# Performance work log

Measured on AMD Instinct MI355X. Metric: run time of the kernel, lower is better.

The kernel has to match this reference:

```python
import jax, jax.numpy as jnp
import numpy as np

ARRAY_SIZE = 128   # crossbar rows
CBITS = 4          # psum ADC bits
LEV = 2 ** (CBITS - 1)
ALPHA = ARRAY_SIZE / LEV   # psum quant step
EPS = 1e-5

# ---- binary activation / weight quant with STE (hardtanh grad) ----
@jax.custom_vjp
def ste_sign(x):
    return jnp.where(x >= 0, 1.0, -1.0).astype(x.dtype)

def _sign_fwd(x):
    return ste_sign(x), x

def _sign_bwd(x, g):
    return (g * (jnp.abs(x) <= 1.0).astype(g.dtype),)

ste_sign.defvjp(_sign_fwd, _sign_bwd)

# ---- psum (partial-sum) quantization: cbits-level ADC over each crossbar array ----
@jax.custom_vjp
def psum_quant(p):
    return jnp.clip(jnp.round(p / ALPHA), -LEV, LEV - 1) * ALPHA

def _pq_fwd(p):
    return psum_quant(p), p

def _pq_bwd(p, g):
    return (g * (jnp.abs(p) <= ARRAY_SIZE).astype(g.dtype),)

psum_quant.defvjp(_pq_fwd, _pq_bwd)

# ---- layers ----
def bn(x, p):
    g, b, m, v = p  # each [C]
    sh = (1, -1) + (1,) * (x.ndim - 2)
    return (x - m.reshape(sh)) * (g.reshape(sh) / jnp.sqrt(v.reshape(sh) + EPS)) + b.reshape(sh)

def maxpool2(x):
    return jax.lax.reduce_window(x, -jnp.inf, jax.lax.max, (1, 1, 2, 2), (1, 1, 2, 2), 'VALID')

def conv_same(x, w):
    return jax.lax.conv_general_dilated(x, w, (1, 1), 'SAME')

def psum_conv(x, w):
    # crossbar-mapped conv: input channels split into groups of arraySize//(kh*kw),
    # each group conv'd separately, psum-quantized (ADC), then accumulated.
    O, Cin, kh, kw = w.shape
    chunk = max(1, ARRAY_SIZE // (kh * kw))
    G = -(-Cin // chunk)
    pad = G * chunk - Cin
    xp = jnp.pad(x, ((0, 0), (0, pad), (0, 0), (0, 0)))
    wp = jnp.pad(w, ((0, 0), (0, pad), (0, 0), (0, 0)))
    B, _, H, W = x.shape
    xg = xp.reshape(B, G, chunk, H, W).transpose(1, 0, 2, 3, 4)   # [G,B,c,H,W]
    wg = wp.reshape(O, G, chunk, kh, kw).transpose(1, 0, 2, 3, 4)  # [G,O,c,kh,kw]
    ps = jax.vmap(conv_same)(xg, wg)                               # [G,B,O,H,W]
    return psum_quant(ps).sum(0)

def psum_linear(x, w):
    # x [B,D], w [O,D]; D divisible by ARRAY_SIZE
    B, D = x.shape
    O = w.shape[0]
    G = D // ARRAY_SIZE
    ps = jnp.einsum('bgc,ogc->gbo', x.reshape(B, G, ARRAY_SIZE), w.reshape(O, G, ARRAY_SIZE))
    return psum_quant(ps).sum(0)


def setup_inputs() -> dict:
    key = jax.random.key(0)
    ks = iter(jax.random.split(key, 64))
    def nrm(shape, s=0.05):
        return jax.random.normal(next(ks), shape, jnp.float32) * s
    def bnp(C):
        return jnp.stack([jax.random.uniform(next(ks), (C,), jnp.float32) + 0.5,
                          nrm((C,), 0.1), nrm((C,), 0.1),
                          jax.random.uniform(next(ks), (C,), jnp.float32) + 0.5])
    return dict(
        x=jax.random.normal(next(ks), (64, 3, 32, 32), jnp.float32),
        conv0_w=nrm((128, 3, 3, 3)), bn0=bnp(128),
        w1=nrm((128, 128, 3, 3)), bn1=bnp(128),
        w2=nrm((256, 128, 3, 3)), bn2=bnp(256),
        w3=nrm((256, 256, 3, 3)), bn3=bnp(256),
        w4=nrm((512, 256, 3, 3)), bn4=bnp(512),
        w5=nrm((512, 512, 3, 3)), bn5=bnp(512),
        fc1_w=nrm((1024, 8192)), bnf1=bnp(1024),
        fc2_w=nrm((1024, 1024)), bnf2=bnp(1024),
        out_w=nrm((10, 1024)), out_b=nrm((10,)), bnout=bnp(10),
    )


def reference(x, conv0_w, bn0, w1, bn1, w2, bn2, w3, bn3, w4, bn4, w5, bn5,
              fc1_w, bnf1, fc2_w, bnf2, out_w, out_b, bnout):
    h = conv_same(x, conv0_w)                       # full-precision first conv
    h = ste_sign(bn(h, bn0))
    h = psum_conv(h, ste_sign(w1)); h = maxpool2(h); h = ste_sign(bn(h, bn1))
    h = psum_conv(h, ste_sign(w2)); h = ste_sign(bn(h, bn2))
    h = psum_conv(h, ste_sign(w3)); h = maxpool2(h); h = ste_sign(bn(h, bn3))
    h = psum_conv(h, ste_sign(w4)); h = ste_sign(bn(h, bn4))
    h = psum_conv(h, ste_sign(w5)); h = maxpool2(h); h = ste_sign(bn(h, bn5))
    h = h.reshape(h.shape[0], -1)                   # [B, 8192]
    h = ste_sign(bn(psum_linear(h, ste_sign(fc1_w)), bnf1))
    h = bn(psum_linear(h, ste_sign(fc2_w)), bnf2)   # abits=32 -> identity nonlinear
    h = h @ out_w.T + out_b
    return bn(h, bnout)
```

## Files before the change

kernel.cpp:

```cpp
#include <hip/hip_runtime.h>
#include <cstdint>
#include <cstddef>

using bf16x8 = __attribute__((ext_vector_type(8))) short;
using f32x4  = __attribute__((ext_vector_type(4))) float;
using u32x4  = __attribute__((ext_vector_type(4))) unsigned int;

#define DI __device__ __forceinline__

DI float pq3(float a) {
    return fminf(rintf(a), 7.f);
}
DI float pq16(float ps) {
    return fminf(rintf(ps * 0.0625f), 7.f) * 16.f;
}

DI float bnv(float x, float g, float b, float m, float v) {
    return (x - m) * (g / sqrtf(v + 1e-5f)) + b;
}

DI unsigned short sgn_bf16(float v) {
    return (v >= 0.f) ? (unsigned short)0x3F80 : (unsigned short)0xBF80;
}

__global__ __launch_bounds__(256)
void k_conv0(const float* __restrict__ x, const float* __restrict__ w,
             const float* __restrict__ bnp, unsigned short* __restrict__ out) {
    __shared__ float sX[3][3][36];
    const int b = blockIdx.x >> 5, y = blockIdx.x & 31;
    const int tid = threadIdx.x;
    const int o = tid & 127, xc = tid >> 7;

    for (int i = tid; i < 3 * 3 * 36; i += 256) {
        int col = i % 36, rr = (i / 36) % 3, c = i / 108;
        int gy = y + rr - 1, gx = col - 1;
        float v = 0.f;
        if ((unsigned)gy < 32u && (unsigned)gx < 32u)
            v = x[((b * 3 + c) * 32 + gy) * 32 + gx];
        sX[c][rr][col] = v;
    }
    float wr[27];
    const float* wp = w + o * 27;
    #pragma unroll
    for (int t = 0; t < 27; ++t) wr[t] = wp[t];
    __syncthreads();

    const float bg = bnp[o], bb = bnp[128 + o], bm = bnp[256 + o], bv = bnp[384 + o];
    unsigned short* op = out + ((size_t)(b * 32 + y) * 32) * 128 + o;

    #pragma unroll
    for (int q = 0; q < 4; ++q) {
        float acc0 = 0.f, acc1 = 0.f, acc2 = 0.f, acc3 = 0.f;
        const int X0 = xc * 16 + q * 4;
        #pragma unroll
        for (int c = 0; c < 3; ++c)
            #pragma unroll
            for (int ky = 0; ky < 3; ++ky) {
                float xv0 = sX[c][ky][X0 + 0], xv1 = sX[c][ky][X0 + 1];
                float xv2 = sX[c][ky][X0 + 2], xv3 = sX[c][ky][X0 + 3];
                float xv4 = sX[c][ky][X0 + 4], xv5 = sX[c][ky][X0 + 5];
                float w0 = wr[c * 9 + ky * 3 + 0];
                float w1 = wr[c * 9 + ky * 3 + 1];
                float w2 = wr[c * 9 + ky * 3 + 2];
                acc0 += xv0 * w0 + xv1 * w1 + xv2 * w2;
                acc1 += xv1 * w0 + xv2 * w1 + xv3 * w2;
                acc2 += xv2 * w0 + xv3 * w1 + xv4 * w2;
                acc3 += xv3 * w0 + xv4 * w1 + xv5 * w2;
            }
        op[(size_t)(X0 + 0) * 128] = sgn_bf16(bnv(acc0, bg, bb, bm, bv));
        op[(size_t)(X0 + 1) * 128] = sgn_bf16(bnv(acc1, bg, bb, bm, bv));
        op[(size_t)(X0 + 2) * 128] = sgn_bf16(bnv(acc2, bg, bb, bm, bv));
        op[(size_t)(X0 + 3) * 128] = sgn_bf16(bnv(acc3, bg, bb, bm, bv));
    }
}

__global__ __launch_bounds__(256)
void k_pack_w(const float* __restrict__ w, unsigned short* __restrict__ wpk,
              int Cin, int O, int G) {
    int idx = blockIdx.x * 256 + threadIdx.x;
    int total = G * O * 160;
    if (idx >= total) return;
    int c = idx & 15;
    int tap = (idx >> 4) % 10;
    int rest = idx / 160;
    int o = rest % O, g = rest / O;
    unsigned short v = 0;
    int cg = g * 14 + c;
    if (tap < 9 && c < 14 && cg < Cin)
        v = (w[((size_t)o * Cin + cg) * 9 + tap] >= 0.f) ? (unsigned short)0x3D80
                                                         : (unsigned short)0xBD80;
    wpk[idx] = v;
}

template <int H, int W, int Cin, int O, int G, int RH, int RW, int POOLMODE>
__global__ __launch_bounds__(256)
void k_conv_mfma(const unsigned int* __restrict__ act,
                 const unsigned short* __restrict__ wpk,
                 const float* __restrict__ bnp,
                 unsigned short* __restrict__ outa,
                 unsigned short* __restrict__ a5p,
                 const unsigned int* __restrict__ zbuf) {
    constexpr int SH = RH + 2, SW = RW + 2;
    constexpr int MS = RH * RW / 16;
    constexpr int NREGX = W / RW;
    constexpr int SLOT8 = SH * SW * 8;
    constexpr int NST = (SLOT8 + 255) / 256;
    static_assert(POOLMODE != 1 || RW == 16, "pool mode 1 needs RW=16");
    static_assert(POOLMODE != 2 || (RW == 8 && MS == 4), "pool mode 2 needs 8x8");

    __shared__ __align__(16) unsigned int sA[SH * SW * 12];

    const int tid  = threadIdx.x;
    const int regY = (int)blockIdx.x / NREGX, regX = (int)blockIdx.x % NREGX;
    const int o0   = blockIdx.y * 64;
    const int b    = blockIdx.z;

    const int lane = tid & 63, wv = tid >> 6;
    const int n  = lane & 15;
    const int kb = lane >> 4;
    const int hb = kb >> 1, ch = kb & 1;

    const unsigned int* sptr[NST];
    int sdst[NST];
    #pragma unroll
    for (int it = 0; it < NST; ++it) {
        int i = it * 256 + tid;
        sdst[it] = -1;
        if (i < SLOT8) {
            int cp = i & 7, slot = i >> 3;
            int yy = slot / SW, xx = slot - yy * SW;
            int gy = regY * RH + yy - 1, gx = regX * RW + xx - 1;
            sdst[it] = slot * 12 + (((cp >> 2) + slot) % 3) * 4 + (cp & 3);
            sptr[it] = ((unsigned)gy < (unsigned)H && (unsigned)gx < (unsigned)W)
                     ? act + ((size_t)(b * H + gy) * W + gx) * (Cin / 2) + cp
                     : zbuf + cp;
        }
    }

    int offMS[MS][5];
    #pragma unroll
    for (int ms = 0; ms < MS; ++ms) {
        int p = ms * 16 + n;
        int y = p / RW, x = p % RW;
        #pragma unroll
        for (int s = 0; s < 5; ++s) {
            int t = 2 * s + hb;
            int slotT = (t <= 8) ? ((y + t / 3) * SW + (x + t % 3)) : (y * SW + x);
            offMS[ms][s] = slotT * 48 + ((ch + slotT) % 3) * 16;
        }
    }

    float tot[MS][4];
    #pragma unroll
    for (int ms = 0; ms < MS; ++ms) {
        tot[ms][0] = 0.f; tot[ms][1] = 0.f; tot[ms][2] = 0.f; tot[ms][3] = 0.f;
    }

    const unsigned short* wg = wpk + ((size_t)o0 + wv * 16 + n) * 160 + ch * 8;

    #pragma unroll 1
    for (int g = 0; g < G; ++g) {
        #pragma unroll
        for (int it = 0; it < NST; ++it)
            if (sdst[it] >= 0) {
                sA[sdst[it]] = *sptr[it];
                sptr[it] += 7;
            }
        bf16x8 bq[5];
        #pragma unroll
        for (int s = 0; s < 5; ++s) {
            int tap = 2 * s + hb;
            bq[s] = *(const bf16x8*)(wg + tap * 16);
        }
        wg += O * 160;
        __syncthreads();

        const char* sAc = (const char*)sA;
        #pragma unroll
        for (int ms = 0; ms < MS; ++ms) {
            f32x4 acc = {0.f, 0.f, 0.f, 0.f};
            #pragma unroll
            for (int s = 0; s < 5; ++s) {
                bf16x8 af = *(const bf16x8*)(sAc + offMS[ms][s]);
                acc = __builtin_amdgcn_mfma_f32_16x16x32_bf16(af, bq[s], acc, 0, 0, 0);
            }
            tot[ms][0] += pq3(acc[0]);
            tot[ms][1] += pq3(acc[1]);
            tot[ms][2] += pq3(acc[2]);
            tot[ms][3] += pq3(acc[3]);
        }
        __syncthreads();
    }

    const int oc = o0 + wv * 16 + n;
    const float bg = bnp[oc], bb = bnp[O + oc], bm = bnp[2 * O + oc], bvr = bnp[3 * O + oc];

    if constexpr (POOLMODE == 0) {
        #pragma unroll
        for (int ms = 0; ms < MS; ++ms)
            #pragma unroll
            for (int r = 0; r < 4; ++r) {
                int p = ms * 16 + 4 * kb + r;
                int y = regY * RH + p / RW, x = regX * RW + p % RW;
                float val = bnv(16.f * tot[ms][r], bg, bb, bm, bvr);
                outa[(((size_t)b * H + y) * W + x) * O + oc] = sgn_bf16(val);
            }
    } else if constexpr (POOLMODE == 1) {
        #pragma unroll
        for (int j = 0; j < MS / 2; ++j)
            #pragma unroll
            for (int q = 0; q < 2; ++q) {
                float v = fmaxf(fmaxf(tot[2 * j][2 * q], tot[2 * j][2 * q + 1]),
                                fmaxf(tot[2 * j + 1][2 * q], tot[2 * j + 1][2 * q + 1]));
                float val = bnv(16.f * v, bg, bb, bm, bvr);
                int py = regY * (RH / 2) + j, px = regX * (RW / 2) + 2 * kb + q;
                outa[(((size_t)b * (H / 2) + py) * (W / 2) + px) * O + oc] = sgn_bf16(val);
            }
    } else {
        #pragma unroll
        for (int ms = 0; ms < MS; ++ms)
            #pragma unroll
            for (int q = 0; q < 2; ++q) {
                float h = fmaxf(tot[ms][2 * q], tot[ms][2 * q + 1]);
                float o2 = __shfl_xor(h, 32);
                float v = fmaxf(h, o2);
                if (hb == 0) {
                    float val = bnv(16.f * v, bg, bb, bm, bvr);
                    int d = oc * 16 + ms * 4 + 2 * ch + q;
                    a5p[((size_t)(d >> 3) * 64 + b) * 8 + (d & 7)] = sgn_bf16(val);
                }
            }
    }
}

template <int D, int GPB>
__global__ __launch_bounds__(256)
void k_fc_mfma(const unsigned short* __restrict__ bpk, const float* __restrict__ w,
               float* __restrict__ accg) {
    const int lane = threadIdx.x & 63, wv = threadIdx.x >> 6;
    const int n = lane & 15, kb = lane >> 4;
    const int orow = blockIdx.x * 64 + wv * 16 + n;
    const int g0 = blockIdx.y * GPB;

    float tot[4][4];
    #pragma unroll
    for (int s = 0; s < 4; ++s)
        #pragma unroll
        for (int r = 0; r < 4; ++r) tot[s][r] = 0.f;

    #pragma unroll 1
    for (int g = 0; g < GPB; ++g) {
        const int kbase = (g0 + g) * 128;
        f32x4 a0 = {0,0,0,0}, a1 = {0,0,0,0}, a2 = {0,0,0,0}, a3 = {0,0,0,0};
        #pragma unroll
        for (int s = 0; s < 4; ++s) {
            const int k0 = kbase + s * 32 + kb * 8;
            const float* wp = w + (size_t)orow * D + k0;
            float4 wlo = *(const float4*)wp;
            float4 whi = *(const float4*)(wp + 4);
            bf16x8 af;
            af[0] = (short)sgn_bf16(wlo.x); af[1] = (short)sgn_bf16(wlo.y);
            af[2] = (short)sgn_bf16(wlo.z); af[3] = (short)sgn_bf16(wlo.w);
            af[4] = (short)sgn_bf16(whi.x); af[5] = (short)sgn_bf16(whi.y);
            af[6] = (short)sgn_bf16(whi.z); af[7] = (short)sgn_bf16(whi.w);
            const unsigned short* bp = bpk + (size_t)(k0 >> 3) * 512;
            bf16x8 b0 = *(const bf16x8*)(bp + (n +  0) * 8);
            bf16x8 b1 = *(const bf16x8*)(bp + (n + 16) * 8);
            bf16x8 b2 = *(const bf16x8*)(bp + (n + 32) * 8);
            bf16x8 b3 = *(const bf16x8*)(bp + (n + 48) * 8);
            a0 = __builtin_amdgcn_mfma_f32_16x16x32_bf16(af, b0, a0, 0, 0, 0);
            a1 = __builtin_amdgcn_mfma_f32_16x16x32_bf16(af, b1, a1, 0, 0, 0);
            a2 = __builtin_amdgcn_mfma_f32_16x16x32_bf16(af, b2, a2, 0, 0, 0);
            a3 = __builtin_amdgcn_mfma_f32_16x16x32_bf16(af, b3, a3, 0, 0, 0);
        }
        #pragma unroll
        for (int r = 0; r < 4; ++r) {
            tot[0][r] += pq16(a0[r]); tot[1][r] += pq16(a1[r]);
            tot[2][r] += pq16(a2[r]); tot[3][r] += pq16(a3[r]);
        }
    }
    const int od = blockIdx.x * 64 + wv * 16 + kb * 4;
    #pragma unroll
    for (int s = 0; s < 4; ++s)
        #pragma unroll
        for (int r = 0; r < 4; ++r)
            atomicAdd(&accg[(size_t)(od + r) * 64 + s * 16 + n], tot[s][r]);
}

template <bool SIGN>
__global__ __launch_bounds__(256)
void k_fc_ep(const float* __restrict__ accg, const float* __restrict__ bnp,
             unsigned short* __restrict__ packed, float* __restrict__ h2, int O) {
    int idx = blockIdx.x * 256 + threadIdx.x;
    int b = idx & 63, o = idx >> 6;
    float val = bnv(accg[idx], bnp[o], bnp[O + o], bnp[2 * O + o], bnp[3 * O + o]);
    if (SIGN) packed[((size_t)(o >> 3) * 64 + b) * 8 + (o & 7)] = sgn_bf16(val);
    else      h2[(size_t)b * 1024 + o] = val;
}

__global__ __launch_bounds__(64)
void k_out(const float* __restrict__ h2, const float* __restrict__ ow,
           const float* __restrict__ ob, const float* __restrict__ bnp,
           float* __restrict__ out) {
    int b = blockIdx.x / 10, o = blockIdx.x % 10;
    int lane = threadIdx.x;
    float acc = 0.f;
    #pragma unroll
    for (int i = 0; i < 16; ++i) {
        int k = i * 64 + lane;
        acc += h2[b * 1024 + k] * ow[o * 1024 + k];
    }
    #pragma unroll
    for (int off = 32; off; off >>= 1) acc += __shfl_xor(acc, off);
    if (lane == 0)
        out[b * 10 + o] = bnv(acc + ob[o], bnp[o], bnp[10 + o], bnp[20 + o], bnp[30 + o]);
}

extern "C" void kernel_launch(void* const* d_in, const int* in_sizes, int n_in,
                              void* d_out, int out_size, void* d_ws, size_t ws_size,
                              hipStream_t stream) {
    const float* x     = (const float*)d_in[0];
    const float* w0    = (const float*)d_in[1];
    const float* bn0   = (const float*)d_in[2];
    const float* w1    = (const float*)d_in[3];
    const float* bn1   = (const float*)d_in[4];
    const float* w2    = (const float*)d_in[5];
    const float* bn2   = (const float*)d_in[6];
    const float* w3    = (const float*)d_in[7];
    const float* bn3   = (const float*)d_in[8];
    const float* w4    = (const float*)d_in[9];
    const float* bn4   = (const float*)d_in[10];
    const float* w5    = (const float*)d_in[11];
    const float* bn5   = (const float*)d_in[12];
    const float* fc1w  = (const float*)d_in[13];
    const float* bnf1  = (const float*)d_in[14];
    const float* fc2w  = (const float*)d_in[15];
    const float* bnf2  = (const float*)d_in[16];
    const float* outw  = (const float*)d_in[17];
    const float* outb  = (const float*)d_in[18];
    const float* bnout = (const float*)d_in[19];

    char* ws = (char*)d_ws;
    unsigned short* actA  = (unsigned short*)(ws);
    unsigned short* actB  = (unsigned short*)(ws + 16777216);
    unsigned short* wpk   = (unsigned short*)(ws + 20971520);
    unsigned short* a5p   = (unsigned short*)(ws + 27262976);
    unsigned short* a6p   = (unsigned short*)(ws + 28311552);
    float*          h1acc = (float*)(ws + 28442624);
    float*          h2acc = (float*)(ws + 28704768);
    float*          h2    = (float*)(ws + 28966912);
    unsigned int*   zbuf  = (unsigned int*)(ws + 29229056);

    const unsigned int* actA32 = (const unsigned int*)actA;
    const unsigned int* actB32 = (const unsigned int*)actB;

    hipMemsetAsync(h1acc, 0, 262144, stream);
    hipMemsetAsync(h2acc, 0, 262144, stream);
    hipMemsetAsync(zbuf, 0, 4096, stream);

    k_conv0<<<dim3(2048), dim3(256), 0, stream>>>(x, w0, bn0, actA);

    k_pack_w<<<dim3(800), dim3(256), 0, stream>>>(w1, wpk, 128, 128, 10);
    k_conv_mfma<32, 32, 128, 128, 10, 4, 16, 1>
        <<<dim3(16, 2, 64), dim3(256), 0, stream>>>(actA32, wpk, bn1, actB, nullptr, zbuf);

    k_pack_w<<<dim3(1600), dim3(256), 0, stream>>>(w2, wpk, 128, 256, 10);
    k_conv_mfma<16, 16, 128, 256, 10, 4, 16, 0>
        <<<dim3(4, 4, 64), dim3(256), 0, stream>>>(actB32, wpk, bn2, actA, nullptr, zbuf);

    k_pack_w<<<dim3(3040), dim3(256), 0, stream>>>(w3, wpk, 256, 256, 19);
    k_conv_mfma<16, 16, 256, 256, 19, 4, 16, 1>
        <<<dim3(4, 4, 64), dim3(256), 0, stream>>>(actA32, wpk, bn3, actB, nullptr, zbuf);

    k_pack_w<<<dim3(6080), dim3(256), 0, stream>>>(w4, wpk, 256, 512, 19);
    k_conv_mfma<8, 8, 256, 512, 19, 8, 8, 0>
        <<<dim3(1, 8, 64), dim3(256), 0, stream>>>(actB32, wpk, bn4, actA, nullptr, zbuf);

    k_pack_w<<<dim3(11840), dim3(256), 0, stream>>>(w5, wpk, 512, 512, 37);
    k_conv_mfma<8, 8, 512, 512, 37, 8, 8, 2>
        <<<dim3(1, 8, 64), dim3(256), 0, stream>>>(actA32, wpk, bn5, nullptr, a5p, zbuf);

    k_fc_mfma<8192, 1><<<dim3(16, 64), dim3(256), 0, stream>>>(a5p, fc1w, h1acc);
    k_fc_ep<true><<<dim3(256), dim3(256), 0, stream>>>(h1acc, bnf1, a6p, nullptr, 1024);
    k_fc_mfma<1024, 1><<<dim3(16, 8), dim3(256), 0, stream>>>(a6p, fc2w, h2acc);
    k_fc_ep<false><<<dim3(256), dim3(256), 0, stream>>>(h2acc, bnf2, nullptr, h2, 1024);
    k_out<<<dim3(640), dim3(64), 0, stream>>>(h2, outw, outb, bnout, (float*)d_out);
}
```

Before: 285.8 us.

## Split conv MFMA warp work 2x2 over spatial and channels, repack weights coalesced

```diff
diff --git a/kernel.cpp b/kernel.cpp
--- a/kernel.cpp
+++ b/kernel.cpp
@@ -75,17 +75,16 @@
 }
 
 __global__ __launch_bounds__(256)
-void k_pack_w(const float* __restrict__ w, unsigned short* __restrict__ wpk,
-              int Cin, int O, int G) {
+void k_pack_w2(const float* __restrict__ w, unsigned short* __restrict__ wpk,
+               int Cin, int O, int G) {
     int idx = blockIdx.x * 256 + threadIdx.x;
-    int total = G * O * 160;
-    if (idx >= total) return;
-    int c = idx & 15;
-    int tap = (idx >> 4) % 10;
-    int rest = idx / 160;
-    int o = rest % O, g = rest / O;
+    if (idx >= G * O * 160) return;
+    int c8 = idx & 7;
+    int o  = (idx >> 3) % O;
+    int r2 = (idx >> 3) / O;
+    int chdw = r2 & 1, tap = (r2 >> 1) % 10, g = r2 / 20;
+    int c = chdw * 8 + c8, cg = g * 14 + c;
     unsigned short v = 0;
-    int cg = g * 14 + c;
     if (tap < 9 && c < 14 && cg < Cin)
         v = (w[((size_t)o * Cin + cg) * 9 + tap] >= 0.f) ? (unsigned short)0x3D80
                                                          : (unsigned short)0xBD80;
@@ -95,7 +94,7 @@
 template <int H, int W, int Cin, int O, int G, int RH, int RW, int POOLMODE>
 __global__ __launch_bounds__(256)
 void k_conv_mfma(const unsigned int* __restrict__ act,
-                 const unsigned short* __restrict__ wpk,
+                 const char* __restrict__ wpk2,
                  const float* __restrict__ bnp,
                  unsigned short* __restrict__ outa,
                  unsigned short* __restrict__ a5p,
@@ -105,8 +104,9 @@
     constexpr int NREGX = W / RW;
     constexpr int SLOT8 = SH * SW * 8;
     constexpr int NST = (SLOT8 + 255) / 256;
+    static_assert(MS == 4, "2x2 decomposition needs MS==4");
     static_assert(POOLMODE != 1 || RW == 16, "pool mode 1 needs RW=16");
-    static_assert(POOLMODE != 2 || (RW == 8 && MS == 4), "pool mode 2 needs 8x8");
+    static_assert(POOLMODE != 2 || RW == 8, "pool mode 2 needs 8x8");
 
     __shared__ __align__(16) unsigned int sA[SH * SW * 12];
 
@@ -119,6 +119,8 @@
     const int n  = lane & 15;
     const int kb = lane >> 4;
     const int hb = kb >> 1, ch = kb & 1;
+    const int mp = wv & 1;
+    const int oh = wv >> 1;
 
     const unsigned int* sptr[NST];
     int sdst[NST];
@@ -137,26 +139,28 @@
         }
     }
 
-    int offMS[MS][5];
-    #pragma unroll
-    for (int ms = 0; ms < MS; ++ms) {
-        int p = ms * 16 + n;
+    int offMS[2][5];
+    #pragma unroll
+    for (int j = 0; j < 2; ++j) {
+        int p = (2 * mp + j) * 16 + n;
         int y = p / RW, x = p % RW;
         #pragma unroll
         for (int s = 0; s < 5; ++s) {
             int t = 2 * s + hb;
             int slotT = (t <= 8) ? ((y + t / 3) * SW + (x + t % 3)) : (y * SW + x);
-            offMS[ms][s] = slotT * 48 + ((ch + slotT) % 3) * 16;
-        }
-    }
-
-    float tot[MS][4];
-    #pragma unroll
-    for (int ms = 0; ms < MS; ++ms) {
-        tot[ms][0] = 0.f; tot[ms][1] = 0.f; tot[ms][2] = 0.f; tot[ms][3] = 0.f;
-    }
-
-    const unsigned short* wg = wpk + ((size_t)o0 + wv * 16 + n) * 160 + ch * 8;
+            offMS[j][s] = slotT * 48 + ((ch + slotT) % 3) * 16;
+        }
+    }
+
+    float tot[2][2][4];
+    #pragma unroll
+    for (int j = 0; j < 2; ++j)
+        #pragma unroll
+        for (int hf = 0; hf < 2; ++hf)
+            #pragma unroll
+            for (int r = 0; r < 4; ++r) tot[j][hf][r] = 0.f;
+
+    const char* wl = wpk2 + (size_t)(o0 + oh * 32 + n) * 16 + (size_t)ch * (O * 16);
 
     #pragma unroll 1
     for (int g = 0; g < G; ++g) {
@@ -166,70 +170,74 @@
                 sA[sdst[it]] = *sptr[it];
                 sptr[it] += 7;
             }
-        bf16x8 bq[5];
+        bf16x8 bq[2][5];
         #pragma unroll
         for (int s = 0; s < 5; ++s) {
-            int tap = 2 * s + hb;
-            bq[s] = *(const bf16x8*)(wg + tap * 16);
-        }
-        wg += O * 160;
+            const char* wt = wl + (size_t)(2 * s + hb) * (2 * O * 16);
+            bq[0][s] = *(const bf16x8*)(wt);
+            bq[1][s] = *(const bf16x8*)(wt + 256);
+        }
+        wl += (size_t)20 * O * 16;
         __syncthreads();
 
         const char* sAc = (const char*)sA;
         #pragma unroll
-        for (int ms = 0; ms < MS; ++ms) {
-            f32x4 acc = {0.f, 0.f, 0.f, 0.f};
+        for (int j = 0; j < 2; ++j) {
+            f32x4 a0 = {0.f, 0.f, 0.f, 0.f}, a1 = {0.f, 0.f, 0.f, 0.f};
             #pragma unroll
             for (int s = 0; s < 5; ++s) {
-                bf16x8 af = *(const bf16x8*)(sAc + offMS[ms][s]);
-                acc = __builtin_amdgcn_mfma_f32_16x16x32_bf16(af, bq[s], acc, 0, 0, 0);
-            }
-            tot[ms][0] += pq3(acc[0]);
-            tot[ms][1] += pq3(acc[1]);
-            tot[ms][2] += pq3(acc[2]);
-            tot[ms][3] += pq3(acc[3]);
+                bf16x8 af = *(const bf16x8*)(sAc + offMS[j][s]);
+                a0 = __builtin_amdgcn_mfma_f32_16x16x32_bf16(af, bq[0][s], a0, 0, 0, 0);
+                a1 = __builtin_amdgcn_mfma_f32_16x16x32_bf16(af, bq[1][s], a1, 0, 0, 0);
+            }
+            #pragma unroll
+            for (int r = 0; r < 4; ++r) {
+                tot[j][0][r] += pq3(a0[r]);
+                tot[j][1][r] += pq3(a1[r]);
+            }
         }
         __syncthreads();
     }
 
-    const int oc = o0 + wv * 16 + n;
-    const float bg = bnp[oc], bb = bnp[O + oc], bm = bnp[2 * O + oc], bvr = bnp[3 * O + oc];
-
-    if constexpr (POOLMODE == 0) {
-        #pragma unroll
-        for (int ms = 0; ms < MS; ++ms)
-            #pragma unroll
-            for (int r = 0; r < 4; ++r) {
-                int p = ms * 16 + 4 * kb + r;
-                int y = regY * RH + p / RW, x = regX * RW + p % RW;
-                float val = bnv(16.f * tot[ms][r], bg, bb, bm, bvr);
-                outa[(((size_t)b * H + y) * W + x) * O + oc] = sgn_bf16(val);
-            }
-    } else if constexpr (POOLMODE == 1) {
-        #pragma unroll
-        for (int j = 0; j < MS / 2; ++j)
+    #pragma unroll
+    for (int hf = 0; hf < 2; ++hf) {
+        const int oc = o0 + oh * 32 + hf * 16 + n;
+        const float bg = bnp[oc], bb = bnp[O + oc], bm = bnp[2 * O + oc], bvr = bnp[3 * O + oc];
+
+        if constexpr (POOLMODE == 0) {
+            #pragma unroll
+            for (int j = 0; j < 2; ++j)
+                #pragma unroll
+                for (int r = 0; r < 4; ++r) {
+                    int p = (2 * mp + j) * 16 + 4 * kb + r;
+                    int y = regY * RH + p / RW, x = regX * RW + p % RW;
+                    float val = bnv(16.f * tot[j][hf][r], bg, bb, bm, bvr);
+                    outa[(((size_t)b * H + y) * W + x) * O + oc] = sgn_bf16(val);
+                }
+        } else if constexpr (POOLMODE == 1) {
             #pragma unroll
             for (int q = 0; q < 2; ++q) {
-                float v = fmaxf(fmaxf(tot[2 * j][2 * q], tot[2 * j][2 * q + 1]),
-                                fmaxf(tot[2 * j + 1][2 * q], tot[2 * j + 1][2 * q + 1]));
+                float v = fmaxf(fmaxf(tot[0][hf][2 * q], tot[0][hf][2 * q + 1]),
+                                fmaxf(tot[1][hf][2 * q], tot[1][hf][2 * q + 1]));
                 float val = bnv(16.f * v, bg, bb, bm, bvr);
-                int py = regY * (RH / 2) + j, px = regX * (RW / 2) + 2 * kb + q;
+                int py = regY * (RH / 2) + mp, px = regX * (RW / 2) + 2 * kb + q;
                 outa[(((size_t)b * (H / 2) + py) * (W / 2) + px) * O + oc] = sgn_bf16(val);
             }
-    } else {
-        #pragma unroll
-        for (int ms = 0; ms < MS; ++ms)
-            #pragma unroll
-            for (int q = 0; q < 2; ++q) {
-                float h = fmaxf(tot[ms][2 * q], tot[ms][2 * q + 1]);
-                float o2 = __shfl_xor(h, 32);
-                float v = fmaxf(h, o2);
-                if (hb == 0) {
-                    float val = bnv(16.f * v, bg, bb, bm, bvr);
-                    int d = oc * 16 + ms * 4 + 2 * ch + q;
-                    a5p[((size_t)(d >> 3) * 64 + b) * 8 + (d & 7)] = sgn_bf16(val);
+        } else {
+            #pragma unroll
+            for (int j = 0; j < 2; ++j)
+                #pragma unroll
+                for (int q = 0; q < 2; ++q) {
+                    float h = fmaxf(tot[j][hf][2 * q], tot[j][hf][2 * q + 1]);
+                    float o2 = __shfl_xor(h, 32);
+                    float v = fmaxf(h, o2);
+                    if (hb == 0) {
+                        float val = bnv(16.f * v, bg, bb, bm, bvr);
+                        int d = oc * 16 + (2 * mp + j) * 4 + 2 * ch + q;
+                        a5p[((size_t)(d >> 3) * 64 + b) * 8 + (d & 7)] = sgn_bf16(val);
+                    }
                 }
-            }
+        }
     }
 }
 
@@ -353,6 +361,7 @@
 
     const unsigned int* actA32 = (const unsigned int*)actA;
     const unsigned int* actB32 = (const unsigned int*)actB;
+    const char* wpkc = (const char*)wpk;
 
     hipMemsetAsync(h1acc, 0, 262144, stream);
     hipMemsetAsync(h2acc, 0, 262144, stream);
@@ -360,25 +369,25 @@
 
     k_conv0<<<dim3(2048), dim3(256), 0, stream>>>(x, w0, bn0, actA);
 
-    k_pack_w<<<dim3(800), dim3(256), 0, stream>>>(w1, wpk, 128, 128, 10);
+    k_pack_w2<<<dim3(800), dim3(256), 0, stream>>>(w1, wpk, 128, 128, 10);
     k_conv_mfma<32, 32, 128, 128, 10, 4, 16, 1>
-        <<<dim3(16, 2, 64), dim3(256), 0, stream>>>(actA32, wpk, bn1, actB, nullptr, zbuf);
-
-    k_pack_w<<<dim3(1600), dim3(256), 0, stream>>>(w2, wpk, 128, 256, 10);
+        <<<dim3(16, 2, 64), dim3(256), 0, stream>>>(actA32, wpkc, bn1, actB, nullptr, zbuf);
+
+    k_pack_w2<<<dim3(1600), dim3(256), 0, stream>>>(w2, wpk, 128, 256, 10);
     k_conv_mfma<16, 16, 128, 256, 10, 4, 16, 0>
-        <<<dim3(4, 4, 64), dim3(256), 0, stream>>>(actB32, wpk, bn2, actA, nullptr, zbuf);
-
-    k_pack_w<<<dim3(3040), dim3(256), 0, stream>>>(w3, wpk, 256, 256, 19);
+        <<<dim3(4, 4, 64), dim3(256), 0, stream>>>(actB32, wpkc, bn2, actA, nullptr, zbuf);
+
+    k_pack_w2<<<dim3(3040), dim3(256), 0, stream>>>(w3, wpk, 256, 256, 19);
     k_conv_mfma<16, 16, 256, 256, 19, 4, 16, 1>
-        <<<dim3(4, 4, 64), dim3(256), 0, stream>>>(actA32, wpk, bn3, actB, nullptr, zbuf);
-
-    k_pack_w<<<dim3(6080), dim3(256), 0, stream>>>(w4, wpk, 256, 512, 19);
+        <<<dim3(4, 4, 64), dim3(256), 0, stream>>>(actA32, wpkc, bn3, actB, nullptr, zbuf);
+
+    k_pack_w2<<<dim3(6080), dim3(256), 0, stream>>>(w4, wpk, 256, 512, 19);
     k_conv_mfma<8, 8, 256, 512, 19, 8, 8, 0>
-        <<<dim3(1, 8, 64), dim3(256), 0, stream>>>(actB32, wpk, bn4, actA, nullptr, zbuf);
-
-    k_pack_w<<<dim3(11840), dim3(256), 0, stream>>>(w5, wpk, 512, 512, 37);
+        <<<dim3(1, 8, 64), dim3(256), 0, stream>>>(actB32, wpkc, bn4, actA, nullptr, zbuf);
+
+    k_pack_w2<<<dim3(11840), dim3(256), 0, stream>>>(w5, wpk, 512, 512, 37);
     k_conv_mfma<8, 8, 512, 512, 37, 8, 8, 2>
-        <<<dim3(1, 8, 64), dim3(256), 0, stream>>>(actA32, wpk, bn5, nullptr, a5p, zbuf);
+        <<<dim3(1, 8, 64), dim3(256), 0, stream>>>(actA32, wpkc, bn5, nullptr, a5p, zbuf);
 
     k_fc_mfma<8192, 1><<<dim3(16, 64), dim3(256), 0, stream>>>(a5p, fc1w, h1acc);
     k_fc_ep<true><<<dim3(256), dim3(256), 0, stream>>>(h1acc, bnf1, a6p, nullptr, 1024);
```

Result: faster. 269.2 us (-5.8%).
